# Performance work log

Measured on AMD Instinct MI355X. Metric: run time of the kernel, lower is better.

Reference implementation:

```python
import jax, jax.numpy as jnp
import numpy as np

T, B, D, H = 110, 256, 512, 512
EPS = 1e-9


def _forward(a, v, l, qmask, umask, mu_a, mu_v, mu_l, shifta, shiftv,
             turna, turnb, W1, b1, W2, b2):
    Tcur = a.shape[0]
    # ca = mu * (cos(a) + i sin(a)) = mu * exp(i a)
    ca = mu_a[:Tcur] * jnp.exp(1j * a)          # (T,B,D) complex64
    cv = mu_v[:Tcur] * jnp.exp(1j * v)
    cl = mu_l[:Tcur] * jnp.exp(1j * l)
    # phase shift of a and v streams, then sum into lav
    features = cl + ca * jnp.exp(1j * shifta) + cv * jnp.exp(1j * shiftv)  # (T,B,D)

    # --- step 0 (special-cased in the original loop) ---
    temp0 = features[0]                          # (B,D) complex
    qa0 = qmask[0][:, 0:1]                       # (B,1)
    qb0 = qmask[0][:, 1:2]
    ones = jnp.ones_like(temp0) * (1.0 + 1.0j)   # pA=pB=1+1j initial state
    pA0 = (1.0 - qa0) * ones + qa0 * temp0
    pB0 = (1.0 - qb0) * ones + qb0 * temp0

    # --- steps 1..T-1 as a fused scan over time ---
    def step(carry, xs):
        pA, pB = carry
        f, qm, ta, tb = xs                       # f:(B,D) cplx, qm:(B,2), ta/tb:(1,D)
        qa = qm[:, 0:1]
        qb = qm[:, 1:2]
        turn = qa * (pA * jnp.exp(1j * ta)) + qb * (pB * jnp.exp(1j * tb))
        # torch: turn.where(turn==0, turn/(abs+eps)) -> keep 0 where 0, else normalize
        turn = jnp.where(turn == 0, turn, turn / (jnp.abs(turn) + EPS))
        temp = f + turn
        pA = (1.0 - qa) * pA + qa * temp
        pB = (1.0 - qb) * pB + qb * temp
        return (pA, pB), temp

    (_, _), temps = jax.lax.scan(
        step, (pA0, pB0),
        (features[1:], qmask[1:], turna[1:Tcur], turnb[1:Tcur]))

    feats = jnp.concatenate([temp0[None], temps], axis=0)  # (T,B,D) complex
    fr, fi = feats.real, feats.imag
    f1r = fr @ W1.T + b1
    f1i = fi @ W1.T + b1
    f2r = fr @ W2.T + b2
    f2i = fi @ W2.T + b2
    xr = f1r - f2i
    xi = f1i + f2r
    return xr + xi                               # (T,B,H) float32


def setup_inputs() -> dict:
    key = jax.random.key(0)
    ks = jax.random.split(key, 12)
    a = jax.random.normal(ks[0], (T, B, D), jnp.float32)
    v = jax.random.normal(ks[1], (T, B, D), jnp.float32)
    l = jax.random.normal(ks[2], (T, B, D), jnp.float32)
    spk = jax.random.randint(ks[3], (T, B), 0, 2)
    qmask = jax.nn.one_hot(spk, 2, dtype=jnp.float32)      # (T,B,2)
    umask = jnp.ones((T, B), jnp.float32)                  # unused by forward
    mu_a = jnp.ones((110, 1, 1), jnp.float32)
    mu_v = jnp.ones((110, 1, 1), jnp.float32)
    mu_l = jnp.ones((110, 1, 1), jnp.float32)
    shifta = jax.random.normal(ks[4], (1, 1, D), jnp.float32)
    shiftv = jax.random.normal(ks[5], (1, 1, D), jnp.float32)
    turna = jax.random.uniform(ks[6], (110, 1, D), jnp.float32)
    turnb = jax.random.uniform(ks[7], (110, 1, D), jnp.float32)
    W1 = jax.random.normal(ks[8], (H, D), jnp.float32) * 0.02
    b1 = jnp.zeros((H,), jnp.float32)
    W2 = jax.random.normal(ks[9], (H, D), jnp.float32) * 0.02
    b2 = jnp.zeros((H,), jnp.float32)
    return {"a": a, "v": v, "l": l, "qmask": qmask, "umask": umask,
            "mu_a": mu_a, "mu_v": mu_v, "mu_l": mu_l,
            "shifta": shifta, "shiftv": shiftv,
            "turna": turna, "turnb": turnb,
            "W1": W1, "b1": b1, "W2": W2, "b2": b2,
            "dia_len": T}


def reference(a, v, l, qmask, umask, mu_a, mu_v, mu_l, shifta, shiftv,
              turna, turnb, W1, b1, W2, b2, dia_len):
    return _forward(a, v, l, qmask, umask, mu_a, mu_v, mu_l,
                    shifta, shiftv, turna, turnb, W1, b1, W2, b2)
```

## Files before the change

### kernel.cpp

```cpp
#include <hip/hip_runtime.h>

#define T_DIM 110
#define B_DIM 256
#define D_DIM 512
#define H_DIM 512
#define K_CAT 1024
#define M_DIM (T_DIM * B_DIM)
#define BD    (B_DIM * D_DIM)

typedef float f32x4 __attribute__((ext_vector_type(4)));
typedef short bf16x8 __attribute__((ext_vector_type(8)));

static __device__ __forceinline__ unsigned short f2bf(float f) {
    unsigned u = __builtin_bit_cast(unsigned, f);
    u += 0x7fffu + ((u >> 16) & 1u);
    return (unsigned short)(u >> 16);
}

__global__ __launch_bounds__(256) void prep_all_kernel(
    const float* __restrict__ W1, const float* __restrict__ b1,
    const float* __restrict__ W2,
    const float* __restrict__ turna, const float* __restrict__ turnb,
    unsigned short* __restrict__ Bt,
    float* __restrict__ bias2,
    float4* __restrict__ TT)
{
    int i = blockIdx.x * 256 + threadIdx.x;
    if (i < H_DIM) bias2[i] = 2.0f * b1[i];
    if (i < T_DIM * D_DIM) {
        float s1, c1, s2, c2;
        __sincosf(turna[i], &s1, &c1);
        __sincosf(turnb[i], &s2, &c2);
        TT[i] = make_float4(c1, s1, c2, s2);
    }
    if (i < H_DIM * K_CAT) {
        int h = i / K_CAT;
        int k = i % K_CAT;
        int j = k >> 1;
        float w = (k & 1) ? (W1[h * D_DIM + j] - W2[h * D_DIM + j])
                          : (W1[h * D_DIM + j] + W2[h * D_DIM + j]);
        Bt[i] = f2bf(w);
    }
}

__global__ __launch_bounds__(256, 1) void feat_scan_kernel(
    const float* __restrict__ a, const float* __restrict__ v,
    const float* __restrict__ l, const float* __restrict__ qmask,
    const float* __restrict__ mu_a, const float* __restrict__ mu_v,
    const float* __restrict__ mu_l,
    const float* __restrict__ shifta, const float* __restrict__ shiftv,
    const float4* __restrict__ TT,
    unsigned int* __restrict__ A32)
{
    __shared__ float qm_s[T_DIM], mua_s[T_DIM], muv_s[T_DIM], mul_s[T_DIM];
    const int tx = threadIdx.x;
    const int b  = blockIdx.x >> 1;
    const int d  = ((blockIdx.x & 1) << 8) + tx;
    if (tx < T_DIM) {
        qm_s[tx]  = qmask[(size_t)(tx * B_DIM + b) * 2];
        mua_s[tx] = mu_a[tx];
        muv_s[tx] = mu_v[tx];
        mul_s[tx] = mu_l[tx];
    }
    const float sa = shifta[d];
    const float sv = shiftv[d];
    __syncthreads();

    const size_t gbase = (size_t)b * D_DIM + d;

#define LOADSLOT(SA_, SV_, SL_, ST_, tt_)                                      \
    { const int tc = (tt_) <= T_DIM - 1 ? (tt_) : T_DIM - 1;                   \
      SA_ = a[(size_t)tc * BD + gbase];                                        \
      SV_ = v[(size_t)tc * BD + gbase];                                        \
      SL_ = l[(size_t)tc * BD + gbase];                                        \
      ST_ = TT[(size_t)tc * D_DIM + d]; }

    float  a0,v0,l0, a1,v1,l1, a2,v2,l2, a3,v3,l3;
    float4 t0,t1,t2,t3;
    float  a4,v4,l4, a5,v5,l5, a6,v6,l6, a7,v7,l7;
    float4 t4,t5,t6,t7;

    LOADSLOT(a0,v0,l0,t0, 0)  LOADSLOT(a1,v1,l1,t1, 1)
    LOADSLOT(a2,v2,l2,t2, 2)  LOADSLOT(a3,v3,l3,t3, 3)
    LOADSLOT(a4,v4,l4,t4, 4)  LOADSLOT(a5,v5,l5,t5, 5)
    LOADSLOT(a6,v6,l6,t6, 6)  LOADSLOT(a7,v7,l7,t7, 7)

    float pAr = 1.f, pAi = 1.f, pBr = 1.f, pBi = 1.f;

#define ITER(tt_, SA_, SV_, SL_, ST_)                                          \
    {                                                                          \
        const int t_ = (tt_);                                                  \
        const float qa = qm_s[t_], ma = mua_s[t_],                             \
                    mv = muv_s[t_], ml = mul_s[t_];                            \
        float sA, cA, sV, cV, sL, cL;                                          \
        __sincosf(SA_ + sa, &sA, &cA);                                         \
        __sincosf(SV_ + sv, &sV, &cV);                                         \
        __sincosf(SL_,      &sL, &cL);                                         \
        float fr = ml * cL + ma * cA + mv * cV;                                \
        float fi = ml * sL + ma * sA + mv * sV;                                \
        const bool isA = qa > 0.5f;                                            \
        const float cp = isA ? ST_.x : ST_.z;                                  \
        const float sp = isA ? ST_.y : ST_.w;                                  \
        const float pr = isA ? pAr : pBr;                                      \
        const float pi = isA ? pAi : pBi;                                      \
        const float tr = pr * cp - pi * sp;                                    \
        const float ti = pr * sp + pi * cp;                                    \
        const float gate = (t_ == 0) ? 0.0f : 1.0f;                            \
        const float m2 = fmaxf(tr * tr + ti * ti, 1e-30f);                     \
        const float inv = gate * __builtin_amdgcn_rsqf(m2);                    \
        fr += tr * inv;                                                        \
        fi += ti * inv;                                                        \
        pAr = isA ? fr : pAr;  pAi = isA ? fi : pAi;                           \
        pBr = isA ? pBr : fr;  pBi = isA ? pBi : fi;                           \
        A32[(size_t)(t_ * B_DIM + b) * (K_CAT / 2) + d] =                      \
            (unsigned)f2bf(fr) | ((unsigned)f2bf(fi) << 16);                   \
    }

    for (int g = 0; g < 104; g += 8) {
        ITER(g + 0, a0, v0, l0, t0)
        ITER(g + 1, a1, v1, l1, t1)
        ITER(g + 2, a2, v2, l2, t2)
        ITER(g + 3, a3, v3, l3, t3)
        LOADSLOT(a0,v0,l0,t0, g + 8)
        LOADSLOT(a1,v1,l1,t1, g + 9)
        LOADSLOT(a2,v2,l2,t2, g + 10)
        LOADSLOT(a3,v3,l3,t3, g + 11)
        __builtin_amdgcn_sched_barrier(0x387);

        ITER(g + 4, a4, v4, l4, t4)
        ITER(g + 5, a5, v5, l5, t5)
        ITER(g + 6, a6, v6, l6, t6)
        ITER(g + 7, a7, v7, l7, t7)
        LOADSLOT(a4,v4,l4,t4, g + 12)
        LOADSLOT(a5,v5,l5,t5, g + 13)
        LOADSLOT(a6,v6,l6,t6, g + 14)
        LOADSLOT(a7,v7,l7,t7, g + 15)
        __builtin_amdgcn_sched_barrier(0x387);
    }
    ITER(104, a0, v0, l0, t0)
    ITER(105, a1, v1, l1, t1)
    ITER(106, a2, v2, l2, t2)
    ITER(107, a3, v3, l3, t3)
    ITER(108, a4, v4, l4, t4)
    ITER(109, a5, v5, l5, t5)
#undef ITER
#undef LOADSLOT
}

#define BM 128
#define BN 128
#define BK 64

__global__ __launch_bounds__(256) void gemm_kernel(
    const unsigned short* __restrict__ A,
    const unsigned short* __restrict__ Bt,
    const float* __restrict__ bias2,
    float* __restrict__ C)
{
    __shared__ __align__(16) unsigned short As[BM * BK];
    __shared__ __align__(16) unsigned short Bs[BN * BK];

    const int tid = threadIdx.x;
    const int wave = tid >> 6;
    const int lane = tid & 63;
    const int wr = wave >> 1;
    const int wc = wave & 1;
    const int m0 = blockIdx.x * BM;
    const int n0 = blockIdx.y * BN;
    const int lrow = lane & 15;
    const int lk8 = (lane >> 4) * 8;

    const int srow = wave * 32;
    const int lrow8 = lane >> 3;
    const int lchunk = lane & 7;

    f32x4 acc[4][4] = {};

    for (int k0 = 0; k0 < K_CAT; k0 += BK) {
        #pragma unroll
        for (int c = 0; c < 4; ++c) {
            const int row = srow + c * 8 + lrow8;
            {
                const unsigned short* gp = A + (size_t)(m0 + row) * K_CAT + k0 + lchunk * 8;
                unsigned short* lp = As + (srow + c * 8) * BK + lane * 8;
                __builtin_amdgcn_global_load_lds(
                    (const __attribute__((address_space(1))) unsigned int*)gp,
                    (__attribute__((address_space(3))) unsigned int*)lp,
                    16, 0, 0);
            }
            {
                const unsigned short* gp = Bt + (size_t)(n0 + row) * K_CAT + k0 + lchunk * 8;
                unsigned short* lp = Bs + (srow + c * 8) * BK + lane * 8;
                __builtin_amdgcn_global_load_lds(
                    (const __attribute__((address_space(1))) unsigned int*)gp,
                    (__attribute__((address_space(3))) unsigned int*)lp,
                    16, 0, 0);
            }
        }
        __syncthreads();

        bf16x8 af[4][2], bfv[4][2];
        #pragma unroll
        for (int m = 0; m < 4; ++m)
            #pragma unroll
            for (int kk = 0; kk < 2; ++kk)
                af[m][kk] = *reinterpret_cast<const bf16x8*>(
                    &As[(wr * 64 + m * 16 + lrow) * BK + kk * 32 + lk8]);
        #pragma unroll
        for (int n = 0; n < 4; ++n)
            #pragma unroll
            for (int kk = 0; kk < 2; ++kk)
                bfv[n][kk] = *reinterpret_cast<const bf16x8*>(
                    &Bs[(wc * 64 + n * 16 + lrow) * BK + kk * 32 + lk8]);

        #pragma unroll
        for (int kk = 0; kk < 2; ++kk)
            #pragma unroll
            for (int m = 0; m < 4; ++m)
                #pragma unroll
                for (int n = 0; n < 4; ++n)
                    acc[m][n] = __builtin_amdgcn_mfma_f32_16x16x32_bf16(
                        af[m][kk], bfv[n][kk], acc[m][n], 0, 0, 0);
        __syncthreads();
    }

    const int rbase = m0 + wr * 64 + (lane >> 4) * 4;
    const int cbase = n0 + wc * 64;
    #pragma unroll
    for (int n = 0; n < 4; ++n) {
        const int col = cbase + n * 16 + lrow;
        const float bv = bias2[col];
        #pragma unroll
        for (int m = 0; m < 4; ++m) {
            const int row0 = rbase + m * 16;
            #pragma unroll
            for (int r = 0; r < 4; ++r) {
                C[(size_t)(row0 + r) * H_DIM + col] = acc[m][n][r] + bv;
            }
        }
    }
}

extern "C" void kernel_launch(void* const* d_in, const int* in_sizes, int n_in,
                              void* d_out, int out_size, void* d_ws, size_t ws_size,
                              hipStream_t stream) {
    const float* a      = (const float*)d_in[0];
    const float* v      = (const float*)d_in[1];
    const float* l      = (const float*)d_in[2];
    const float* qmask  = (const float*)d_in[3];
    const float* mu_a   = (const float*)d_in[5];
    const float* mu_v   = (const float*)d_in[6];
    const float* mu_l   = (const float*)d_in[7];
    const float* shifta = (const float*)d_in[8];
    const float* shiftv = (const float*)d_in[9];
    const float* turna  = (const float*)d_in[10];
    const float* turnb  = (const float*)d_in[11];
    const float* W1     = (const float*)d_in[12];
    const float* b1     = (const float*)d_in[13];
    const float* W2     = (const float*)d_in[14];
    float* out = (float*)d_out;

    char* ws = (char*)d_ws;
    unsigned short* Afeat = (unsigned short*)ws;
    size_t offB  = (size_t)M_DIM * K_CAT * sizeof(unsigned short);
    unsigned short* Bt = (unsigned short*)(ws + offB);
    size_t offBias = offB + (size_t)H_DIM * K_CAT * sizeof(unsigned short);
    float* bias2 = (float*)(ws + offBias);
    size_t offTT = offBias + 4096;
    float4* TT = (float4*)(ws + offTT);

    prep_all_kernel<<<(H_DIM * K_CAT + 255) / 256, 256, 0, stream>>>(
        W1, b1, W2, turna, turnb, Bt, bias2, TT);
    feat_scan_kernel<<<B_DIM * 2, 256, 0, stream>>>(
        a, v, l, qmask, mu_a, mu_v, mu_l, shifta, shiftv, TT, (unsigned int*)Afeat);
    dim3 grid(M_DIM / BM, H_DIM / BN);
    gemm_kernel<<<grid, 256, 0, stream>>>(Afeat, Bt, bias2, out);
}
```

Before: 112.2 us.

## Split feature computation into a fully parallel kernel ahead of the scan

The sincos feature computation moves out of the serial time scan into a separate fully parallel kernel. That kernel writes fp16-packed complex features into the GEMM A buffer, and the scan reads them back and overwrites them in place with bf16 results. This removes transcendental work and three fp32 input streams from the latency-bound scan, which runs only 512 blocks, and spreads that work over many more threads. The cost is an extra launch, a full write and reread of the intermediate buffer, and fp16 rounding of the features before the scan.

```diff
diff --git a/kernel.cpp b/kernel.cpp
--- a/kernel.cpp
+++ b/kernel.cpp
@@ -15,6 +15,12 @@
     unsigned u = __builtin_bit_cast(unsigned, f);
     u += 0x7fffu + ((u >> 16) & 1u);
     return (unsigned short)(u >> 16);
+}
+static __device__ __forceinline__ unsigned short f2h(float f) {
+    return __builtin_bit_cast(unsigned short, (_Float16)f);
+}
+static __device__ __forceinline__ float h2f(unsigned short h) {
+    return (float)__builtin_bit_cast(_Float16, h);
 }
 
 __global__ __launch_bounds__(256) void prep_all_kernel(
@@ -43,62 +49,84 @@
     }
 }
 
-__global__ __launch_bounds__(256, 1) void feat_scan_kernel(
+__global__ __launch_bounds__(256) void feat_kernel(
     const float* __restrict__ a, const float* __restrict__ v,
-    const float* __restrict__ l, const float* __restrict__ qmask,
+    const float* __restrict__ l,
     const float* __restrict__ mu_a, const float* __restrict__ mu_v,
     const float* __restrict__ mu_l,
     const float* __restrict__ shifta, const float* __restrict__ shiftv,
+    unsigned int* __restrict__ A32)
+{
+    const int tid = blockIdx.x * 256 + threadIdx.x;
+    const int row = tid >> 8;
+    const int d2  = (tid & 255) << 1;
+    const int t   = row >> 8;
+    const size_t g = (size_t)row * D_DIM + d2;
+
+    const float2 av = *reinterpret_cast<const float2*>(a + g);
+    const float2 vv = *reinterpret_cast<const float2*>(v + g);
+    const float2 lv = *reinterpret_cast<const float2*>(l + g);
+    const float2 sa = *reinterpret_cast<const float2*>(shifta + d2);
+    const float2 sv = *reinterpret_cast<const float2*>(shiftv + d2);
+    const float ma = mu_a[t], mv = mu_v[t], ml = mu_l[t];
+
+    uint2 outw;
+    {
+        float sA, cA, sV, cV, sL, cL;
+        __sincosf(av.x + sa.x, &sA, &cA);
+        __sincosf(vv.x + sv.x, &sV, &cV);
+        __sincosf(lv.x,        &sL, &cL);
+        const float fr = ml * cL + ma * cA + mv * cV;
+        const float fi = ml * sL + ma * sA + mv * sV;
+        outw.x = (unsigned)f2h(fr) | ((unsigned)f2h(fi) << 16);
+    }
+    {
+        float sA, cA, sV, cV, sL, cL;
+        __sincosf(av.y + sa.y, &sA, &cA);
+        __sincosf(vv.y + sv.y, &sV, &cV);
+        __sincosf(lv.y,        &sL, &cL);
+        const float fr = ml * cL + ma * cA + mv * cV;
+        const float fi = ml * sL + ma * sA + mv * sV;
+        outw.y = (unsigned)f2h(fr) | ((unsigned)f2h(fi) << 16);
+    }
+    *reinterpret_cast<uint2*>(A32 + (size_t)row * (K_CAT / 2) + d2) = outw;
+}
+
+__global__ __launch_bounds__(256, 1) void scan_kernel(
+    const float* __restrict__ qmask,
     const float4* __restrict__ TT,
     unsigned int* __restrict__ A32)
 {
-    __shared__ float qm_s[T_DIM], mua_s[T_DIM], muv_s[T_DIM], mul_s[T_DIM];
+    __shared__ float qm_s[T_DIM];
     const int tx = threadIdx.x;
     const int b  = blockIdx.x >> 1;
     const int d  = ((blockIdx.x & 1) << 8) + tx;
-    if (tx < T_DIM) {
-        qm_s[tx]  = qmask[(size_t)(tx * B_DIM + b) * 2];
-        mua_s[tx] = mu_a[tx];
-        muv_s[tx] = mu_v[tx];
-        mul_s[tx] = mu_l[tx];
-    }
-    const float sa = shifta[d];
-    const float sv = shiftv[d];
+    if (tx < T_DIM) qm_s[tx] = qmask[(size_t)(tx * B_DIM + b) * 2];
     __syncthreads();
 
-    const size_t gbase = (size_t)b * D_DIM + d;
-
-#define LOADSLOT(SA_, SV_, SL_, ST_, tt_)                                      \
+#define AIDX(t_) ((size_t)((t_) * B_DIM + b) * (K_CAT / 2) + d)
+
+#define LOADSLOT(FP_, ST_, tt_)                                                \
     { const int tc = (tt_) <= T_DIM - 1 ? (tt_) : T_DIM - 1;                   \
-      SA_ = a[(size_t)tc * BD + gbase];                                        \
-      SV_ = v[(size_t)tc * BD + gbase];                                        \
-      SL_ = l[(size_t)tc * BD + gbase];                                        \
+      FP_ = A32[AIDX(tc)];                                                     \
       ST_ = TT[(size_t)tc * D_DIM + d]; }
 
-    float  a0,v0,l0, a1,v1,l1, a2,v2,l2, a3,v3,l3;
-    float4 t0,t1,t2,t3;
-    float  a4,v4,l4, a5,v5,l5, a6,v6,l6, a7,v7,l7;
-    float4 t4,t5,t6,t7;
-
-    LOADSLOT(a0,v0,l0,t0, 0)  LOADSLOT(a1,v1,l1,t1, 1)
-    LOADSLOT(a2,v2,l2,t2, 2)  LOADSLOT(a3,v3,l3,t3, 3)
-    LOADSLOT(a4,v4,l4,t4, 4)  LOADSLOT(a5,v5,l5,t5, 5)
-    LOADSLOT(a6,v6,l6,t6, 6)  LOADSLOT(a7,v7,l7,t7, 7)
+    unsigned f0, f1, f2, f3, f4, f5, f6, f7;
+    float4   t0, t1, t2, t3, t4, t5, t6, t7;
+
+    LOADSLOT(f0, t0, 0)  LOADSLOT(f1, t1, 1)
+    LOADSLOT(f2, t2, 2)  LOADSLOT(f3, t3, 3)
+    LOADSLOT(f4, t4, 4)  LOADSLOT(f5, t5, 5)
+    LOADSLOT(f6, t6, 6)  LOADSLOT(f7, t7, 7)
 
     float pAr = 1.f, pAi = 1.f, pBr = 1.f, pBi = 1.f;
 
-#define ITER(tt_, SA_, SV_, SL_, ST_)                                          \
+#define ITER(tt_, FP_, ST_)                                                    \
     {                                                                          \
         const int t_ = (tt_);                                                  \
-        const float qa = qm_s[t_], ma = mua_s[t_],                             \
-                    mv = muv_s[t_], ml = mul_s[t_];                            \
-        float sA, cA, sV, cV, sL, cL;                                          \
-        __sincosf(SA_ + sa, &sA, &cA);                                         \
-        __sincosf(SV_ + sv, &sV, &cV);                                         \
-        __sincosf(SL_,      &sL, &cL);                                         \
-        float fr = ml * cL + ma * cA + mv * cV;                                \
-        float fi = ml * sL + ma * sA + mv * sV;                                \
-        const bool isA = qa > 0.5f;                                            \
+        float fr = h2f((unsigned short)(FP_ & 0xffffu));                       \
+        float fi = h2f((unsigned short)(FP_ >> 16));                           \
+        const bool isA = qm_s[t_] > 0.5f;                                      \
         const float cp = isA ? ST_.x : ST_.z;                                  \
         const float sp = isA ? ST_.y : ST_.w;                                  \
         const float pr = isA ? pAr : pBr;                                      \
@@ -112,39 +140,39 @@
         fi += ti * inv;                                                        \
         pAr = isA ? fr : pAr;  pAi = isA ? fi : pAi;                           \
         pBr = isA ? pBr : fr;  pBi = isA ? pBi : fi;                           \
-        A32[(size_t)(t_ * B_DIM + b) * (K_CAT / 2) + d] =                      \
-            (unsigned)f2bf(fr) | ((unsigned)f2bf(fi) << 16);                   \
+        A32[AIDX(t_)] = (unsigned)f2bf(fr) | ((unsigned)f2bf(fi) << 16);       \
     }
 
     for (int g = 0; g < 104; g += 8) {
-        ITER(g + 0, a0, v0, l0, t0)
-        ITER(g + 1, a1, v1, l1, t1)
-        ITER(g + 2, a2, v2, l2, t2)
-        ITER(g + 3, a3, v3, l3, t3)
-        LOADSLOT(a0,v0,l0,t0, g + 8)
-        LOADSLOT(a1,v1,l1,t1, g + 9)
-        LOADSLOT(a2,v2,l2,t2, g + 10)
-        LOADSLOT(a3,v3,l3,t3, g + 11)
+        ITER(g + 0, f0, t0)
+        ITER(g + 1, f1, t1)
+        ITER(g + 2, f2, t2)
+        ITER(g + 3, f3, t3)
+        LOADSLOT(f0, t0, g + 8)
+        LOADSLOT(f1, t1, g + 9)
+        LOADSLOT(f2, t2, g + 10)
+        LOADSLOT(f3, t3, g + 11)
         __builtin_amdgcn_sched_barrier(0x387);
 
-        ITER(g + 4, a4, v4, l4, t4)
-        ITER(g + 5, a5, v5, l5, t5)
-        ITER(g + 6, a6, v6, l6, t6)
-        ITER(g + 7, a7, v7, l7, t7)
-        LOADSLOT(a4,v4,l4,t4, g + 12)
-        LOADSLOT(a5,v5,l5,t5, g + 13)
-        LOADSLOT(a6,v6,l6,t6, g + 14)
-        LOADSLOT(a7,v7,l7,t7, g + 15)
+        ITER(g + 4, f4, t4)
+        ITER(g + 5, f5, t5)
+        ITER(g + 6, f6, t6)
+        ITER(g + 7, f7, t7)
+        LOADSLOT(f4, t4, g + 12)
+        LOADSLOT(f5, t5, g + 13)
+        LOADSLOT(f6, t6, g + 14)
+        LOADSLOT(f7, t7, g + 15)
         __builtin_amdgcn_sched_barrier(0x387);
     }
-    ITER(104, a0, v0, l0, t0)
-    ITER(105, a1, v1, l1, t1)
-    ITER(106, a2, v2, l2, t2)
-    ITER(107, a3, v3, l3, t3)
-    ITER(108, a4, v4, l4, t4)
-    ITER(109, a5, v5, l5, t5)
+    ITER(104, f0, t0)
+    ITER(105, f1, t1)
+    ITER(106, f2, t2)
+    ITER(107, f3, t3)
+    ITER(108, f4, t4)
+    ITER(109, f5, t5)
 #undef ITER
 #undef LOADSLOT
+#undef AIDX
 }
 
 #define BM 128
@@ -271,8 +299,10 @@
 
     prep_all_kernel<<<(H_DIM * K_CAT + 255) / 256, 256, 0, stream>>>(
         W1, b1, W2, turna, turnb, Bt, bias2, TT);
-    feat_scan_kernel<<<B_DIM * 2, 256, 0, stream>>>(
-        a, v, l, qmask, mu_a, mu_v, mu_l, shifta, shiftv, TT, (unsigned int*)Afeat);
+    feat_kernel<<<(M_DIM * D_DIM / 2) / 256, 256, 0, stream>>>(
+        a, v, l, mu_a, mu_v, mu_l, shifta, shiftv, (unsigned int*)Afeat);
+    scan_kernel<<<B_DIM * 2, 256, 0, stream>>>(
+        qmask, TT, (unsigned int*)Afeat);
     dim3 grid(M_DIM / BM, H_DIM / BN);
     gemm_kernel<<<grid, 256, 0, stream>>>(Afeat, Bt, bias2, out);
 }
```

Measured after the change: 126.1 us. +12.4%, slower.
